# Kernel tuning notes

Measured on AMD Instinct MI355X. Metric: run time of the kernel, lower is better.

The kernel has to match this reference:

```python
import jax, jax.numpy as jnp
import numpy as np

SMOOTH = 9.0   # self.labmda
EPS = 1e-8
MASK_VAL = -1.0

I, R, D = 64, 36, 1024   # n_image, n_regions, d
C, W = 64, 32            # n_caption, max_n_word


def setup_inputs() -> dict:
    key = jax.random.key(0)
    k1, k2, k3, k4 = jax.random.split(key, 4)
    imgs = jax.random.normal(k1, (I, R, D), dtype=jnp.float32)
    caps = jax.random.normal(k2, (C, W, D), dtype=jnp.float32)
    img_lens = jax.random.randint(k3, (I,), 1, R + 1)
    cap_lens = jnp.maximum(jax.random.randint(k4, (C,), 0, W + 1), 4)
    return {"imgs": imgs, "caps": caps, "img_lens": img_lens, "cap_lens": cap_lens}


def reference(imgs, caps, img_lens, cap_lens):
    # imgs: (I,R,D) images/regions; caps: (C,W,D); cap_lens: (C,)
    # Vectorized over captions: padded word positions are masked so the
    # per-caption word-dim l2norm matches the ragged torch loop exactly.
    wmask = jnp.arange(W)[None, :] < cap_lens[:, None]          # (C,W)
    wmask_f = wmask.astype(imgs.dtype)

    # attn[c,i,w,r] = <caps[c,w], imgs[i,r]>  (torch: bmm(context, queryT))
    attn = jnp.einsum('ird,cwd->ciwr', imgs, caps)              # (C,I,W,R)
    attn = jax.nn.leaky_relu(attn, 0.1)
    attn = attn * wmask_f[:, None, :, None]                     # zero padded words
    # l2norm over word dim (torch l2norm(attn, 2) on (I,R,W)): eps after sqrt
    norm_w = jnp.sqrt(jnp.sum(attn * attn, axis=2, keepdims=True)) + EPS
    attn = attn / norm_w
    # temperature-scaled softmax over regions
    attn = jax.nn.softmax(attn * SMOOTH, axis=3)                # (C,I,W,R)

    # weighted context per word, l2-normalized over feature dim
    wctx = jnp.einsum('ciwr,ird->ciwd', attn, imgs)             # (C,I,W,D)
    wctx = wctx / (jnp.sqrt(jnp.sum(wctx * wctx, axis=-1, keepdims=True)) + EPS)

    # cosine similarity between the word and its attended context
    cap_e = caps[:, None, :, :]                                 # (C,1,W,D)
    w12 = jnp.sum(cap_e * wctx, axis=-1)                        # (C,I,W)
    w1 = jnp.sqrt(jnp.sum(cap_e * cap_e, axis=-1))
    w2 = jnp.sqrt(jnp.sum(wctx * wctx, axis=-1))
    sim = w12 / jnp.maximum(w1 * w2, EPS)                       # (C,I,W)

    sim = jnp.where(wmask[:, None, :], sim, MASK_VAL)
    return jnp.transpose(sim, (1, 0, 2))                        # (I,C,W)
```

## Files before the change

kernel.cpp:

```cpp
#include <hip/hip_runtime.h>
#include <hip/hip_bf16.h>

#define IDIM 64
#define RDIM 36
#define DDIM 1024
#define CDIM 64
#define WDIM 32
#define SMOOTH 9.0f
#define EPSF 1e-8f

typedef __bf16 bf16_t;
typedef __bf16 bf16x8 __attribute__((ext_vector_type(8)));
typedef __bf16 bf16x4 __attribute__((ext_vector_type(4)));
typedef float f32x4 __attribute__((ext_vector_type(4)));

#define MFMA16(a, b, c) __builtin_amdgcn_mfma_f32_16x16x32_bf16((a), (b), (c), 0, 0, 0)

#define IMGSB_OFF 0
#define IMGSB_BYTES (IDIM * 4 * 8 * 3 * 512 * 2)
#define CAPSA_OFF (IMGSB_OFF + IMGSB_BYTES)
#define CAPSA_BYTES (CDIM * 4 * 8 * 2 * 512 * 2)
#define GF_OFF    (CAPSA_OFF + CAPSA_BYTES)
#define GF_BYTES  (IDIM * 384 * 8 * 2)
#define CAPN_OFF  (GF_OFF + GF_BYTES)

__global__ __launch_bounds__(256) void prep_kernel(
    const float* __restrict__ imgs, const float* __restrict__ caps,
    bf16_t* __restrict__ imgsB, bf16_t* __restrict__ capsA) {
  __shared__ __align__(16) bf16_t ldsb[36 * 264];
  int b = blockIdx.x, tid = threadIdx.x;
  if (b < 256) {
    int i = b >> 2, wvk = b & 3, ks = wvk * 256;
    const float* src = imgs + (size_t)i * RDIM * DDIM + ks;
#pragma unroll
    for (int rep = 0; rep < 9; ++rep) {
      int idx = rep * 256 + tid;
      int row = idx >> 6, q = idx & 63;
      float4 v = *(const float4*)(src + (size_t)row * DDIM + q * 4);
      bf16x4 p;
      p[0] = (bf16_t)v.x; p[1] = (bf16_t)v.y; p[2] = (bf16_t)v.z; p[3] = (bf16_t)v.w;
      *(bf16x4*)&ldsb[row * 264 + q * 4] = p;
    }
    __syncthreads();
    bf16_t* dst = imgsB + (size_t)(i * 4 + wvk) * 12288;
#pragma unroll
    for (int rep = 0; rep < 6; ++rep) {
      int u = rep * 256 + tid;
      int kk = u / 192, rem = u - kk * 192;
      int nt = rem >> 6, lane = rem & 63, qd = lane >> 4, l15 = lane & 15;
      int row = nt * 16 + l15;
      bf16x8 p;
      if (row < 36) {
        p = *(const bf16x8*)&ldsb[row * 264 + kk * 32 + qd * 8];
      } else {
#pragma unroll
        for (int j = 0; j < 8; ++j) p[j] = (bf16_t)0.0f;
      }
      *(bf16x8*)(dst + (size_t)u * 8) = p;
    }
  } else {
    int bb = b - 256;
    int c = bb >> 2, wvk = bb & 3, ks = wvk * 256;
    const float* src = caps + (size_t)c * WDIM * DDIM + ks;
#pragma unroll
    for (int rep = 0; rep < 8; ++rep) {
      int idx = rep * 256 + tid;
      int row = idx >> 6, q = idx & 63;
      float4 v = *(const float4*)(src + (size_t)row * DDIM + q * 4);
      bf16x4 p;
      p[0] = (bf16_t)v.x; p[1] = (bf16_t)v.y; p[2] = (bf16_t)v.z; p[3] = (bf16_t)v.w;
      *(bf16x4*)&ldsb[row * 264 + q * 4] = p;
    }
    __syncthreads();
    bf16_t* dst = capsA + (size_t)(c * 4 + wvk) * 8192;
#pragma unroll
    for (int rep = 0; rep < 4; ++rep) {
      int u = rep * 256 + tid;
      int kk = u >> 7, rem = u & 127;
      int mt = rem >> 6, lane = rem & 63, qd = lane >> 4, l15 = lane & 15;
      int row = mt * 16 + l15;
      bf16x8 p = *(const bf16x8*)&ldsb[row * 264 + kk * 32 + qd * 8];
      *(bf16x8*)(dst + (size_t)u * 8) = p;
    }
  }
}

__global__ __launch_bounds__(256) void gram_kernel(
    const bf16_t* __restrict__ imgsB, const bf16_t* __restrict__ capsA,
    bf16_t* __restrict__ Gfrag, float* __restrict__ capnorm) {
  __shared__ float part[4][48][49];
  __shared__ float cnl[4][32];
  int bx = blockIdx.x;
  int tid = threadIdx.x, wv = tid >> 6, ln = tid & 63;
  int l15 = ln & 15, qd = ln >> 4;
  if (bx < 64) {
    int i = bx;
    const bf16_t* base = imgsB + (size_t)(i * 4 + wv) * 12288;
    f32x4 acc[3][3];
#pragma unroll
    for (int mt = 0; mt < 3; ++mt)
#pragma unroll
      for (int nt = 0; nt < 3; ++nt) {
        f32x4 zf = {0.f, 0.f, 0.f, 0.f};
        acc[mt][nt] = zf;
      }
#pragma unroll
    for (int kk = 0; kk < 8; ++kk) {
      bf16x8 a[3];
#pragma unroll
      for (int nt = 0; nt < 3; ++nt)
        a[nt] = *(const bf16x8*)(base + ((size_t)(kk * 3 + nt) * 64 + ln) * 8);
#pragma unroll
      for (int mt = 0; mt < 3; ++mt)
#pragma unroll
        for (int nt = 0; nt < 3; ++nt)
          acc[mt][nt] = MFMA16(a[mt], a[nt], acc[mt][nt]);
    }
#pragma unroll
    for (int mt = 0; mt < 3; ++mt)
#pragma unroll
      for (int nt = 0; nt < 3; ++nt)
#pragma unroll
        for (int rg = 0; rg < 4; ++rg)
          part[wv][mt * 16 + qd * 4 + rg][nt * 16 + l15] = acc[mt][nt][rg];
    __syncthreads();
    for (int idx = tid; idx < 384; idx += 256) {
      int kk = idx / 192;
      int rem = idx - kk * 192;
      int nt = rem >> 6, lnn = rem & 63;
      int qd2 = lnn >> 4, l152 = lnn & 15;
      int n = nt * 16 + l152;
      bf16x8 pk;
#pragma unroll
      for (int j = 0; j < 8; ++j) {
        int k = kk * 32 + qd2 * 8 + j;
        float v = (k < 48) ? (part[0][k][n] + part[1][k][n] + part[2][k][n] + part[3][k][n]) : 0.f;
        pk[j] = (bf16_t)v;
      }
      *(bf16x8*)(Gfrag + ((size_t)i * 384 + idx) * 8) = pk;
    }
  } else {
    int c = bx - 64;
    const bf16_t* base = capsA + (size_t)(c * 4 + wv) * 8192;
    float ss0 = 0.f, ss1 = 0.f;
#pragma unroll
    for (int kk = 0; kk < 8; ++kk) {
      bf16x8 p0 = *(const bf16x8*)(base + ((size_t)(kk * 2 + 0) * 64 + ln) * 8);
      bf16x8 p1 = *(const bf16x8*)(base + ((size_t)(kk * 2 + 1) * 64 + ln) * 8);
#pragma unroll
      for (int j = 0; j < 8; ++j) {
        float v0 = (float)p0[j], v1 = (float)p1[j];
        ss0 += v0 * v0;
        ss1 += v1 * v1;
      }
    }
    ss0 += __shfl_xor(ss0, 16, 64); ss0 += __shfl_xor(ss0, 32, 64);
    ss1 += __shfl_xor(ss1, 16, 64); ss1 += __shfl_xor(ss1, 32, 64);
    if (qd == 0) { cnl[wv][l15] = ss0; cnl[wv][16 + l15] = ss1; }
    __syncthreads();
    if (tid < 32)
      capnorm[c * 32 + tid] = sqrtf(cnl[0][tid] + cnl[1][tid] + cnl[2][tid] + cnl[3][tid]);
  }
}

__global__ __launch_bounds__(256, 4) void main_kernel(
    const bf16_t* __restrict__ capsA, const bf16_t* __restrict__ imgsB,
    const bf16_t* __restrict__ Gfrag, const float* __restrict__ capnorm,
    const int* __restrict__ cap_lens, float* __restrict__ out) {
  __shared__ __align__(16) bf16_t attnS[4][32 * 72];

  int bx = blockIdx.x;
  int wv = threadIdx.x >> 6, ln = threadIdx.x & 63;
  int l15 = ln & 15, qd = ln >> 4;
  int xcd = bx & 7, t = bx >> 3;
  int c = t & 63, ih = t >> 6;
  int i = xcd * 8 + ih * 4 + wv;
  int clen = cap_lens[c];

  const bf16_t* Ab = capsA + (size_t)c * (4 * 8 * 2 * 512);
  const bf16_t* Bb = imgsB + (size_t)i * (4 * 8 * 3 * 512);

  f32x4 acc[2][3];
#pragma unroll
  for (int mt = 0; mt < 2; ++mt)
#pragma unroll
    for (int nt = 0; nt < 3; ++nt) {
      f32x4 zf = {0.f, 0.f, 0.f, 0.f};
      acc[mt][nt] = zf;
    }
#pragma unroll 4
  for (int s = 0; s < 32; ++s) {
    const bf16_t* ap = Ab + (size_t)s * 1024 + ln * 8;
    const bf16_t* bp = Bb + (size_t)s * 1536 + ln * 8;
    bf16x8 a0 = *(const bf16x8*)(ap);
    bf16x8 a1 = *(const bf16x8*)(ap + 512);
    bf16x8 b0 = *(const bf16x8*)(bp);
    bf16x8 b1 = *(const bf16x8*)(bp + 512);
    bf16x8 b2 = *(const bf16x8*)(bp + 1024);
    acc[0][0] = MFMA16(a0, b0, acc[0][0]);
    acc[0][1] = MFMA16(a0, b1, acc[0][1]);
    acc[0][2] = MFMA16(a0, b2, acc[0][2]);
    acc[1][0] = MFMA16(a1, b0, acc[1][0]);
    acc[1][1] = MFMA16(a1, b1, acc[1][1]);
    acc[1][2] = MFMA16(a1, b2, acc[1][2]);
  }

  const bf16_t* Gb = Gfrag + (size_t)i * 3072;
  bf16x8 ga[2][3];
#pragma unroll
  for (int kk = 0; kk < 2; ++kk)
#pragma unroll
    for (int nt = 0; nt < 3; ++nt)
      ga[kk][nt] = *(const bf16x8*)(Gb + ((size_t)(kk * 3 + nt) * 64 + ln) * 8);

  float sinv[3];
#pragma unroll
  for (int nt = 0; nt < 3; ++nt) {
    bool padn = (nt == 2) && (l15 >= 4);
    float ns = 0.f;
#pragma unroll
    for (int mt = 0; mt < 2; ++mt)
#pragma unroll
      for (int rg = 0; rg < 4; ++rg) {
        float v = acc[mt][nt][rg];
        float l = (v > 0.f) ? v : 0.1f * v;
        int m = mt * 16 + qd * 4 + rg;
        if (m >= clen || padn) l = 0.f;
        ns += l * l;
      }
    ns += __shfl_xor(ns, 16, 64);
    ns += __shfl_xor(ns, 32, 64);
    sinv[nt] = SMOOTH / (sqrtf(ns) + EPSF);
  }

  float Srow[2][4];
#pragma unroll
  for (int mt = 0; mt < 2; ++mt)
#pragma unroll
    for (int rg = 0; rg < 4; ++rg) {
      int m = mt * 16 + qd * 4 + rg;
      bool mrow = (m >= clen);
      float z[3];
#pragma unroll
      for (int nt = 0; nt < 3; ++nt) {
        float v = acc[mt][nt][rg];
        float l = (v > 0.f) ? v : 0.1f * v;
        if (mrow) l = 0.f;
        float zz = l * sinv[nt];
        if (nt == 2 && l15 >= 4) zz = -1e30f;
        z[nt] = zz;
      }
      float mx = fmaxf(fmaxf(z[0], z[1]), z[2]);
#pragma unroll
      for (int off = 1; off < 16; off <<= 1) mx = fmaxf(mx, __shfl_xor(mx, off, 64));
      float e[3], es = 0.f;
#pragma unroll
      for (int nt = 0; nt < 3; ++nt) {
        e[nt] = __expf(z[nt] - mx);
        es += e[nt];
      }
#pragma unroll
      for (int off = 1; off < 16; off <<= 1) es += __shfl_xor(es, off, 64);
      float inv = 1.0f / es;
      float sac = 0.f;
#pragma unroll
      for (int nt = 0; nt < 3; ++nt) {
        float a = e[nt] * inv;
        sac += a * acc[mt][nt][rg];
        acc[mt][nt][rg] = a;
      }
#pragma unroll
      for (int off = 1; off < 16; off <<= 1) sac += __shfl_xor(sac, off, 64);
      Srow[mt][rg] = sac;
    }

  bf16_t* as = &attnS[wv][0];
#pragma unroll
  for (int mt = 0; mt < 2; ++mt)
#pragma unroll
    for (int nt = 0; nt < 3; ++nt)
#pragma unroll
      for (int rg = 0; rg < 4; ++rg)
        as[(mt * 16 + qd * 4 + rg) * 72 + nt * 16 + l15] = (bf16_t)acc[mt][nt][rg];
  {
    bf16x8 z8;
#pragma unroll
    for (int q = 0; q < 8; ++q) z8[q] = (bf16_t)0.0f;
    *(bf16x8*)(as + (ln >> 1) * 72 + 48 + (ln & 1) * 8) = z8;
  }
  bf16x8 fa[2][2];
#pragma unroll
  for (int mt = 0; mt < 2; ++mt)
#pragma unroll
    for (int kk = 0; kk < 2; ++kk)
      fa[mt][kk] = *(const bf16x8*)(as + (mt * 16 + l15) * 72 + kk * 32 + qd * 8);

  f32x4 y[2][3];
#pragma unroll
  for (int mt = 0; mt < 2; ++mt)
#pragma unroll
    for (int nt = 0; nt < 3; ++nt) {
      f32x4 zf = {0.f, 0.f, 0.f, 0.f};
      y[mt][nt] = zf;
    }
#pragma unroll
  for (int kk = 0; kk < 2; ++kk)
#pragma unroll
    for (int mt = 0; mt < 2; ++mt)
#pragma unroll
      for (int nt = 0; nt < 3; ++nt)
        y[mt][nt] = MFMA16(fa[mt][kk], ga[kk][nt], y[mt][nt]);

  float n2row[2][4];
#pragma unroll
  for (int mt = 0; mt < 2; ++mt)
#pragma unroll
    for (int rg = 0; rg < 4; ++rg) {
      float nn = 0.f;
#pragma unroll
      for (int nt = 0; nt < 3; ++nt) nn += y[mt][nt][rg] * acc[mt][nt][rg];
#pragma unroll
      for (int off = 1; off < 16; off <<= 1) nn += __shfl_xor(nn, off, 64);
      n2row[mt][rg] = nn;
    }

  if (l15 < 2) {
    int mt = l15;
    f32x4 cn = *(const f32x4*)(capnorm + c * 32 + mt * 16 + qd * 4);
    f32x4 o;
#pragma unroll
    for (int rg = 0; rg < 4; ++rg) {
      float n2v = fmaxf(n2row[mt][rg], 0.f);
      float nrm = sqrtf(n2v);
      float den = nrm + EPSF;
      float w12 = Srow[mt][rg] / den;
      float w2 = nrm / den;
      float sim = w12 / fmaxf(cn[rg] * w2, EPSF);
      int m = mt * 16 + qd * 4 + rg;
      if (m >= clen) sim = -1.0f;
      o[rg] = sim;
    }
    *(f32x4*)(out + ((size_t)i * CDIM + c) * WDIM + mt * 16 + qd * 4) = o;
  }
}

extern "C" void kernel_launch(void* const* d_in, const int* in_sizes, int n_in,
                              void* d_out, int out_size, void* d_ws, size_t ws_size,
                              hipStream_t stream) {
  const float* imgs = (const float*)d_in[0];
  const float* caps = (const float*)d_in[1];
  const int* cap_lens = (const int*)d_in[3];
  float* out = (float*)d_out;

  char* ws = (char*)d_ws;
  bf16_t* imgsB = (bf16_t*)(ws + IMGSB_OFF);
  bf16_t* capsA = (bf16_t*)(ws + CAPSA_OFF);
  bf16_t* Gfrag = (bf16_t*)(ws + GF_OFF);
  float* capnorm = (float*)(ws + CAPN_OFF);

  prep_kernel<<<512, 256, 0, stream>>>(imgs, caps, imgsB, capsA);
  gram_kernel<<<128, 256, 0, stream>>>(imgsB, capsA, Gfrag, capnorm);
  main_kernel<<<1024, 256, 0, stream>>>(capsA, imgsB, Gfrag, capnorm, cap_lens, out);
}
```

Measured before the change: 106.1 us.

## Share image tile across caption waves via double-buffered LDS staging

Changes the block mapping so each block holds one image and four captions (one per wave) rather than one caption and four images. The image's B fragments are loaded cooperatively into a double-buffered LDS tile and shared by all four waves, with the next chunk prefetched into registers while the current chunk is consumed. This cuts redundant global loads of image data but adds a block-wide barrier per chunk, plus LDS traffic. The attention scratch buffer now reuses the same LDS allocation.

New measurement: 100.7 us. 1.05x faster.

```diff
diff --git a/kernel.cpp b/kernel.cpp
--- a/kernel.cpp
+++ b/kernel.cpp
@@ -167,18 +167,32 @@
     const bf16_t* __restrict__ capsA, const bf16_t* __restrict__ imgsB,
     const bf16_t* __restrict__ Gfrag, const float* __restrict__ capnorm,
     const int* __restrict__ cap_lens, float* __restrict__ out) {
-  __shared__ __align__(16) bf16_t attnS[4][32 * 72];
+  __shared__ __align__(16) bf16_t ldsB[2][6144];
 
   int bx = blockIdx.x;
   int wv = threadIdx.x >> 6, ln = threadIdx.x & 63;
   int l15 = ln & 15, qd = ln >> 4;
-  int xcd = bx & 7, t = bx >> 3;
-  int c = t & 63, ih = t >> 6;
-  int i = xcd * 8 + ih * 4 + wv;
+  int xcd = bx & 7, rest = bx >> 3;
+  int ih = rest & 7, cq = rest >> 3;
+  int i = xcd * 8 + ih;
+  int c = cq * 4 + wv;
   int clen = cap_lens[c];
 
-  const bf16_t* Ab = capsA + (size_t)c * (4 * 8 * 2 * 512);
-  const bf16_t* Bb = imgsB + (size_t)i * (4 * 8 * 3 * 512);
+  const bf16_t* Ab = capsA + (size_t)c * 32768;
+  const bf16_t* Bb = imgsB + (size_t)i * 49152;
+
+  bf16x8 t0, t1, t2;
+  {
+    const bf16_t* gp = Bb + wv * 1536 + ln * 8;
+    t0 = *(const bf16x8*)(gp);
+    t1 = *(const bf16x8*)(gp + 512);
+    t2 = *(const bf16x8*)(gp + 1024);
+    bf16_t* lp = &ldsB[0][wv * 1536 + ln * 8];
+    *(bf16x8*)(lp) = t0;
+    *(bf16x8*)(lp + 512) = t1;
+    *(bf16x8*)(lp + 1024) = t2;
+  }
+  __syncthreads();
 
   f32x4 acc[2][3];
 #pragma unroll
@@ -188,21 +202,39 @@
       f32x4 zf = {0.f, 0.f, 0.f, 0.f};
       acc[mt][nt] = zf;
     }
-#pragma unroll 4
-  for (int s = 0; s < 32; ++s) {
-    const bf16_t* ap = Ab + (size_t)s * 1024 + ln * 8;
-    const bf16_t* bp = Bb + (size_t)s * 1536 + ln * 8;
-    bf16x8 a0 = *(const bf16x8*)(ap);
-    bf16x8 a1 = *(const bf16x8*)(ap + 512);
-    bf16x8 b0 = *(const bf16x8*)(bp);
-    bf16x8 b1 = *(const bf16x8*)(bp + 512);
-    bf16x8 b2 = *(const bf16x8*)(bp + 1024);
-    acc[0][0] = MFMA16(a0, b0, acc[0][0]);
-    acc[0][1] = MFMA16(a0, b1, acc[0][1]);
-    acc[0][2] = MFMA16(a0, b2, acc[0][2]);
-    acc[1][0] = MFMA16(a1, b0, acc[1][0]);
-    acc[1][1] = MFMA16(a1, b1, acc[1][1]);
-    acc[1][2] = MFMA16(a1, b2, acc[1][2]);
+
+  for (int ch = 0; ch < 8; ++ch) {
+    int p = ch & 1;
+    if (ch < 7) {
+      const bf16_t* gp = Bb + (ch + 1) * 6144 + wv * 1536 + ln * 8;
+      t0 = *(const bf16x8*)(gp);
+      t1 = *(const bf16x8*)(gp + 512);
+      t2 = *(const bf16x8*)(gp + 1024);
+    }
+#pragma unroll
+    for (int j = 0; j < 4; ++j) {
+      int s = ch * 4 + j;
+      const bf16_t* ap = Ab + (size_t)s * 1024 + ln * 8;
+      bf16x8 a0 = *(const bf16x8*)(ap);
+      bf16x8 a1 = *(const bf16x8*)(ap + 512);
+      const bf16_t* lp = &ldsB[p][j * 1536 + ln * 8];
+      bf16x8 b0 = *(const bf16x8*)(lp);
+      bf16x8 b1 = *(const bf16x8*)(lp + 512);
+      bf16x8 b2 = *(const bf16x8*)(lp + 1024);
+      acc[0][0] = MFMA16(a0, b0, acc[0][0]);
+      acc[0][1] = MFMA16(a0, b1, acc[0][1]);
+      acc[0][2] = MFMA16(a0, b2, acc[0][2]);
+      acc[1][0] = MFMA16(a1, b0, acc[1][0]);
+      acc[1][1] = MFMA16(a1, b1, acc[1][1]);
+      acc[1][2] = MFMA16(a1, b2, acc[1][2]);
+    }
+    if (ch < 7) {
+      bf16_t* lp = &ldsB[1 - p][wv * 1536 + ln * 8];
+      *(bf16x8*)(lp) = t0;
+      *(bf16x8*)(lp + 512) = t1;
+      *(bf16x8*)(lp + 1024) = t2;
+    }
+    __syncthreads();
   }
 
   const bf16_t* Gb = Gfrag + (size_t)i * 3072;
@@ -274,7 +306,7 @@
       Srow[mt][rg] = sac;
     }
 
-  bf16_t* as = &attnS[wv][0];
+  bf16_t* as = &ldsB[0][0] + wv * 2304;
 #pragma unroll
   for (int mt = 0; mt < 2; ++mt)
 #pragma unroll
```
